# Optimization experiments

Hardware: AMD Instinct MI355X
Metric: run time of the kernel (lower is better)

Reference implementation:

```python
import jax, jax.numpy as jnp
import numpy as np

N_NODES = 100000   # number of graph nodes
N_EDGES = 1000000  # number of edges
D_IN = 64          # input feature dim
D_OUT = 64         # output feature dim
N_RELS = 16        # number of relation types


def setup_inputs() -> dict:
    key = jax.random.key(0)
    k1, k2, k3, k4, k5 = jax.random.split(key, 5)
    feat = jax.random.normal(k1, (N_NODES, D_IN), dtype=jnp.float32)
    weight = jax.random.normal(k2, (N_RELS, D_IN, D_OUT), dtype=jnp.float32) * 0.05
    src = jax.random.randint(k3, (N_EDGES,), 0, N_NODES)
    dst = jax.random.randint(k4, (N_EDGES,), 0, N_NODES)
    etypes = jax.random.randint(k5, (N_EDGES,), 0, N_RELS)
    return {"feat": feat, "weight": weight, "src": src, "dst": dst, "etypes": etypes}


def reference(feat, weight, src, dst, etypes):
    # gather source-node features per edge: h = edges.src['h']
    h = feat[src]                                # [E, d_in]
    n_rels = weight.shape[0]
    e, d_out = h.shape[0], weight.shape[2]

    # gather_mm(h, weight, idx_b=etypes): m_e = h_e @ weight[etypes_e]
    # grouped-GEMM realized as R masked dense GEMMs (R is small, fixed);
    # avoids materializing the [E, d_in, d_out] gathered weight tensor.
    def step(m, rw):
        r, w_r = rw
        mask = jnp.where(etypes == r, 1.0, 0.0).astype(h.dtype)  # [E]
        m = m + mask[:, None] * (h @ w_r)                        # [E, d_out]
        return m, None

    m0 = jnp.zeros((e, d_out), dtype=h.dtype)
    m, _ = jax.lax.scan(step, m0, (jnp.arange(n_rels), weight))

    # update_all(..., fn.sum('m', 'h')): scatter-sum messages to dst nodes
    out = jax.ops.segment_sum(m, dst, num_segments=feat.shape[0])  # [N, d_out]
    return out
```

## Files before the change

kernel.cpp:

```cpp
#include <hip/hip_runtime.h>
#include <hip/hip_bf16.h>
#include <stdint.h>

#define NNODES 100000
#define NEDGES 1000000
#define NRELS 16
#define EPB 2048
#define NB ((NEDGES + EPB - 1) / EPB)
#define PADCAP (NEDGES + NRELS * 64)
#define MAXTILES (PADCAP / 64)
#define NDN NNODES
#define BKT 256
#define NBKT ((NDN + BKT - 1) / BKT)

#define FEAT_BLKS 6250
#define W_BLKS 256
#define SETUP_BLKS (FEAT_BLKS + W_BLKS + NB)
#define SCANS_BLKS (1 + (NBKT + 15) / 16)

#define WS_NEED 157070848ull

using short8  = __attribute__((ext_vector_type(8))) short;
using floatx4 = __attribute__((ext_vector_type(4))) float;
using uintx4  = __attribute__((ext_vector_type(4))) unsigned int;

__device__ __forceinline__ unsigned short f2bf(float f) {
    union { float f; uint32_t u; } v; v.f = f;
    uint32_t u = v.u;
    return (unsigned short)((u + 0x7FFFu + ((u >> 16) & 1u)) >> 16);
}
__device__ __forceinline__ float bf2f(uint32_t u16) {
    union { uint32_t u; float f; } v; v.u = u16 << 16;
    return v.f;
}
__device__ __forceinline__ uint32_t pk2(float a, float b) {
    __hip_bfloat162 h = __float22bfloat162_rn(make_float2(a, b));
    union { __hip_bfloat162 h; uint32_t u; } v; v.h = h;
    return v.u;
}

__global__ void k_setup(const float* __restrict__ feat, const float* __restrict__ W,
                        const int* __restrict__ et, const int* __restrict__ dst,
                        unsigned short* __restrict__ featB, unsigned short* __restrict__ Wt,
                        int* __restrict__ hist16, int* __restrict__ hist391) {
    __shared__ int cnt16[16];
    __shared__ int cnt391[NBKT];
    const int b = blockIdx.x;
    if (b < FEAT_BLKS) {
        int i = (b * 256 + threadIdx.x) * 4;
        const float4 f = *(const float4*)(feat + i);
        ushort4 o;
        o.x = f2bf(f.x); o.y = f2bf(f.y); o.z = f2bf(f.z); o.w = f2bf(f.w);
        *(ushort4*)(featB + i) = o;
    } else if (b < FEAT_BLKS + W_BLKS) {
        int t = (b - FEAT_BLKS) * 256 + threadIdx.x;
        int r = t >> 12, n = (t >> 6) & 63, k = t & 63;
        Wt[t] = f2bf(W[(r << 12) + (k << 6) + n]);
    } else {
        const int bb = b - (FEAT_BLKS + W_BLKS);
        if (threadIdx.x < 16) cnt16[threadIdx.x] = 0;
        for (int t = threadIdx.x; t < NBKT; t += 256) cnt391[t] = 0;
        __syncthreads();
        int start = bb * EPB;
        int end = min(NEDGES, start + EPB);
        for (int i = start + threadIdx.x; i < end; i += 256) {
            atomicAdd(&cnt16[et[i]], 1);
            atomicAdd(&cnt391[dst[i] >> 8], 1);
        }
        __syncthreads();
        if (threadIdx.x < 16) hist16[bb * 16 + threadIdx.x] = cnt16[threadIdx.x];
        for (int t = threadIdx.x; t < NBKT; t += 256)
            hist391[bb * NBKT + t] = cnt391[t];
    }
}

__global__ void __launch_bounds__(1024)
k_scans(const int* __restrict__ hist16, int* __restrict__ bbase16,
        int* __restrict__ Pve,
        const int* __restrict__ hist391, int* __restrict__ bbase391,
        int* __restrict__ bstart) {
    int w = threadIdx.x >> 6;
    int lane = threadIdx.x & 63;
    if (blockIdx.x == 0) {
        __shared__ int s_cnt[16];
        __shared__ int s_P[17];
        int carry = 0;
        for (int c = 0; c < NB; c += 64) {
            int idx = c + lane;
            int v = (idx < NB) ? hist16[idx * 16 + w] : 0;
            int x = v;
            #pragma unroll
            for (int off = 1; off < 64; off <<= 1) {
                int y = __shfl_up(x, off);
                if (lane >= off) x += y;
            }
            if (idx < NB) bbase16[idx * 16 + w] = carry + x - v;
            carry += __shfl(x, 63);
        }
        if (lane == 0) s_cnt[w] = carry;
        __syncthreads();
        if (threadIdx.x == 0) {
            int p = 0;
            for (int r = 0; r < 16; ++r) {
                s_P[r] = p;
                Pve[r] = p;
                Pve[17 + r] = p + s_cnt[r];
                p += (s_cnt[r] + 63) & ~63;
            }
            s_P[16] = p;
            Pve[16] = p;
        }
        __syncthreads();
        int pw = s_P[w];
        for (int idx = lane; idx < NB; idx += 64)
            bbase16[idx * 16 + w] += pw;
    } else {
        int b = (blockIdx.x - 1) * 16 + w;
        if (b >= NBKT) return;
        int carry = 0;
        for (int c = 0; c < NB; c += 64) {
            int idx = c + lane;
            int v = (idx < NB) ? hist391[idx * NBKT + b] : 0;
            int x = v;
            #pragma unroll
            for (int off = 1; off < 64; off <<= 1) {
                int y = __shfl_up(x, off);
                if (lane >= off) x += y;
            }
            if (idx < NB) bbase391[idx * NBKT + b] = carry + x - v;
            carry += __shfl(x, 63);
        }
        if (lane == 0) bstart[b] = carry;
    }
}

__global__ void k_bscanB(int* __restrict__ bstart) {
    __shared__ int wtot[8];
    int t = threadIdx.x;
    int v = (t < NBKT) ? bstart[t] : 0;
    int lane = t & 63, w = t >> 6;
    int x = v;
    #pragma unroll
    for (int off = 1; off < 64; off <<= 1) {
        int y = __shfl_up(x, off);
        if (lane >= off) x += y;
    }
    if (lane == 63) wtot[w] = x;
    __syncthreads();
    int woff = 0;
    for (int i = 0; i < w; ++i) woff += wtot[i];
    if (t < NBKT) bstart[t] = woff + x - v;
    if (t == 511) {
        int total = 0;
        for (int i = 0; i < 8; ++i) total += wtot[i];
        bstart[NBKT] = total;
    }
}

__global__ void k_scatter(const int* __restrict__ et, const int* __restrict__ src,
                          const int* __restrict__ dst, const int* __restrict__ bbase16,
                          const int* __restrict__ bbase391, const int* __restrict__ bstart,
                          int* __restrict__ srcS, int* __restrict__ keyE,
                          unsigned short* __restrict__ dnode) {
    __shared__ int base16[16];
    __shared__ int base391[NBKT];
    if (threadIdx.x < 16) base16[threadIdx.x] = bbase16[blockIdx.x * 16 + threadIdx.x];
    for (int t = threadIdx.x; t < NBKT; t += 256)
        base391[t] = bbase391[blockIdx.x * NBKT + t] + bstart[t];
    __syncthreads();
    int start = blockIdx.x * EPB;
    int end = min(NEDGES, start + EPB);
    for (int i = start + threadIdx.x; i < end; i += 256) {
        int r = et[i];
        int pos = atomicAdd(&base16[r], 1);
        srcS[pos] = src[i];
        int d = dst[i];
        int bp = atomicAdd(&base391[d >> 8], 1);
        keyE[bp] = pos;
        dnode[bp] = (unsigned short)(d & 255);
    }
}

__global__ void __launch_bounds__(256)
k_bsort(const unsigned short* __restrict__ dnode, const int* __restrict__ keyE,
        const int* __restrict__ bstart,
        int* __restrict__ keyS, int* __restrict__ dnstart) {
    __shared__ int cnt[256];
    __shared__ int nodebase[256];
    __shared__ int wtot[4];
    const int b = blockIdx.x;
    const int start = bstart[b], end = bstart[b + 1];
    const int t = threadIdx.x;
    cnt[t] = 0;
    __syncthreads();
    for (int e = start + t; e < end; e += 256)
        atomicAdd(&cnt[dnode[e]], 1);
    __syncthreads();
    int v = cnt[t];
    int lane = t & 63, w = t >> 6;
    int x = v;
    #pragma unroll
    for (int off = 1; off < 64; off <<= 1) {
        int y = __shfl_up(x, off);
        if (lane >= off) x += y;
    }
    if (lane == 63) wtot[w] = x;
    __syncthreads();
    int woff = 0;
    for (int i = 0; i < w; ++i) woff += wtot[i];
    nodebase[t] = woff + x - v;
    cnt[t] = 0;
    __syncthreads();
    dnstart[b * 256 + t] = start + nodebase[t];
    if (b == NBKT - 1 && t == 255) dnstart[NBKT * 256] = end;
    for (int e = start + t; e < end; e += 256) {
        int node = dnode[e];
        int rk = atomicAdd(&cnt[node], 1);
        keyS[start + nodebase[node] + rk] = keyE[e];
    }
}

__global__ void __launch_bounds__(256)
k_computeA(const unsigned short* __restrict__ featB,
           const unsigned short* __restrict__ Wt,
           const int* __restrict__ srcS, const int* __restrict__ Pve,
           unsigned short* __restrict__ msgE) {
    __shared__ float lds[4][16 * 68];
    const int w = threadIdx.x >> 6;
    const int t = blockIdx.x * 4 + w;
    const int base = t * 64;
    const int total = Pve[16];
    if (base >= total) return;
    int r = 0;
    while (base >= Pve[r + 1]) ++r;
    const int validEnd = Pve[17 + r];
    const int lane = threadIdx.x & 63;
    const int quad = lane >> 4;
    const int l16 = lane & 15;

    const unsigned short* wr = Wt + (r << 12);
    short8 bfr[4][2];
    #pragma unroll
    for (int tn = 0; tn < 4; ++tn)
        #pragma unroll
        for (int ks = 0; ks < 2; ++ks)
            bfr[tn][ks] = *(const short8*)(wr + ((tn * 16 + l16) << 6) + ks * 32 + quad * 8);

    const int rr = lane >> 2, seg = lane & 3;
    #pragma unroll
    for (int tm = 0; tm < 4; ++tm) {
        int row = base + tm * 16 + l16;
        int s = (row < validEnd) ? srcS[row] : 0;
        const unsigned short* fp = featB + (s << 6) + quad * 8;
        short8 a0 = *(const short8*)(fp);
        short8 a1 = *(const short8*)(fp + 32);
        #pragma unroll
        for (int tn = 0; tn < 4; ++tn) {
            floatx4 c = {0.f, 0.f, 0.f, 0.f};
            c = __builtin_amdgcn_mfma_f32_16x16x32_bf16(a0, bfr[tn][0], c, 0, 0, 0);
            c = __builtin_amdgcn_mfma_f32_16x16x32_bf16(a1, bfr[tn][1], c, 0, 0, 0);
            #pragma unroll
            for (int j = 0; j < 4; ++j)
                lds[w][(quad * 4 + j) * 68 + tn * 16 + l16] = c[j];
        }
        int grow = base + tm * 16 + rr;
        const float* lp = &lds[w][rr * 68 + seg * 16];
        uintx4 o0, o1;
        o0.x = pk2(lp[0],  lp[1]);  o0.y = pk2(lp[2],  lp[3]);
        o0.z = pk2(lp[4],  lp[5]);  o0.w = pk2(lp[6],  lp[7]);
        o1.x = pk2(lp[8],  lp[9]);  o1.y = pk2(lp[10], lp[11]);
        o1.z = pk2(lp[12], lp[13]); o1.w = pk2(lp[14], lp[15]);
        uintx4* op = (uintx4*)(msgE + (size_t)grow * 64 + seg * 16);
        op[0] = o0;
        op[1] = o1;
    }
}

__global__ void __launch_bounds__(256)
k_reduce(const unsigned short* __restrict__ msgE, const int* __restrict__ keyS,
         const int* __restrict__ dnstart, float* __restrict__ out) {
    int n = blockIdx.x * 4 + (threadIdx.x >> 6);
    if (n >= NDN) return;
    int lane = threadIdx.x & 63;
    int start = dnstart[n];
    int end = dnstart[n + 1];
    int c8 = (lane & 7) * 8;
    float a0 = 0.f, a1 = 0.f, a2 = 0.f, a3 = 0.f;
    float a4 = 0.f, a5 = 0.f, a6 = 0.f, a7 = 0.f;
    for (int row = start + (lane >> 3); row < end; row += 8) {
        int rp = keyS[row];
        uintx4 v = *(const uintx4*)(msgE + (size_t)rp * 64 + c8);
        a0 += bf2f(v.x & 0xffffu); a1 += bf2f(v.x >> 16);
        a2 += bf2f(v.y & 0xffffu); a3 += bf2f(v.y >> 16);
        a4 += bf2f(v.z & 0xffffu); a5 += bf2f(v.z >> 16);
        a6 += bf2f(v.w & 0xffffu); a7 += bf2f(v.w >> 16);
    }
    #pragma unroll
    for (int m = 8; m <= 32; m <<= 1) {
        a0 += __shfl_xor(a0, m); a1 += __shfl_xor(a1, m);
        a2 += __shfl_xor(a2, m); a3 += __shfl_xor(a3, m);
        a4 += __shfl_xor(a4, m); a5 += __shfl_xor(a5, m);
        a6 += __shfl_xor(a6, m); a7 += __shfl_xor(a7, m);
    }
    if (lane < 8) {
        float* op = out + (size_t)n * 64 + lane * 8;
        *(float4*)(op)     = make_float4(a0, a1, a2, a3);
        *(float4*)(op + 4) = make_float4(a4, a5, a6, a7);
    }
}

__global__ void __launch_bounds__(256)
k_fb(const float* __restrict__ feat, const float* __restrict__ W,
     const int* __restrict__ src, const int* __restrict__ dst,
     const int* __restrict__ et, float* __restrict__ out) {
    int e = blockIdx.x * 4 + (threadIdx.x >> 6);
    if (e >= NEDGES) return;
    int c = threadIdx.x & 63;
    int s = src[e], d = dst[e], r = et[e];
    const float* fr = feat + (size_t)s * 64;
    const float* wr = W + ((size_t)r << 12);
    float acc = 0.f;
    for (int k = 0; k < 64; ++k) acc += fr[k] * wr[k * 64 + c];
    atomicAdd(out + (size_t)d * 64 + c, acc);
}

extern "C" void kernel_launch(void* const* d_in, const int* in_sizes, int n_in,
                              void* d_out, int out_size, void* d_ws, size_t ws_size,
                              hipStream_t stream) {
    const float* feat = (const float*)d_in[0];
    const float* W    = (const float*)d_in[1];
    const int* src    = (const int*)d_in[2];
    const int* dst    = (const int*)d_in[3];
    const int* et     = (const int*)d_in[4];
    float* out = (float*)d_out;
    char* ws = (char*)d_ws;

    unsigned short* featB = (unsigned short*)(ws);
    unsigned short* Wt    = (unsigned short*)(ws + 12800000);
    int* hist16   = (int*)(ws + 12931072);
    int* bbase16  = (int*)(ws + 12963840);
    int* Pve      = (int*)(ws + 12996608);
    int* hist391  = (int*)(ws + 12996864);
    int* bbase391 = (int*)(ws + 13764864);
    int* bstart   = (int*)(ws + 14532864);
    unsigned short* dnode = (unsigned short*)(ws + 14534912);
    int* dnstart  = (int*)(ws + 16534912);
    int* keyE     = (int*)(ws + 16935680);
    int* keyS     = (int*)(ws + 20935680);
    int* srcS     = (int*)(ws + 24935680);
    unsigned short* msgE = (unsigned short*)(ws + 28939776);

    if (ws_size >= WS_NEED) {
        k_setup<<<SETUP_BLKS, 256, 0, stream>>>(feat, W, et, dst, featB, Wt,
                                                hist16, hist391);
        k_scans<<<SCANS_BLKS, 1024, 0, stream>>>(hist16, bbase16, Pve, hist391,
                                                 bbase391, bstart);
        k_bscanB<<<1, 512, 0, stream>>>(bstart);
        k_scatter<<<NB, 256, 0, stream>>>(et, src, dst, bbase16, bbase391, bstart,
                                          srcS, keyE, dnode);
        k_bsort<<<NBKT, 256, 0, stream>>>(dnode, keyE, bstart, keyS, dnstart);
        k_computeA<<<(MAXTILES + 3) / 4, 256, 0, stream>>>(featB, Wt, srcS, Pve, msgE);
        k_reduce<<<(NDN + 3) / 4, 256, 0, stream>>>(msgE, keyS, dnstart, out);
    } else {
        hipMemsetAsync(d_out, 0, (size_t)out_size * sizeof(float), stream);
        k_fb<<<(NEDGES + 3) / 4, 256, 0, stream>>>(feat, W, src, dst, et, out);
    }
}
```

Before: 235.3 us.

## Sub-sort edges by source bucket within each relation for gather locality

Edges are now grouped by relation and, within each relation, by 256-node source bucket. The edge histogram and scatter use a composite key, and the scan stage is restructured to compute the per-bucket offsets. The aim is more cache locality for the feature gathers in the grouped GEMM. In exchange, the histograms grow much larger, EPB doubles to shrink them, and the scan and scatter work increases.

```diff
diff --git a/kernel.cpp b/kernel.cpp
--- a/kernel.cpp
+++ b/kernel.cpp
@@ -5,20 +5,23 @@
 #define NNODES 100000
 #define NEDGES 1000000
 #define NRELS 16
-#define EPB 2048
+#define EPB 4096
 #define NB ((NEDGES + EPB - 1) / EPB)
 #define PADCAP (NEDGES + NRELS * 64)
 #define MAXTILES (PADCAP / 64)
 #define NDN NNODES
 #define BKT 256
 #define NBKT ((NDN + BKT - 1) / BKT)
+#define NSB 391
+#define NCB (NRELS * NSB)
 
 #define FEAT_BLKS 6250
 #define W_BLKS 256
 #define SETUP_BLKS (FEAT_BLKS + W_BLKS + NB)
-#define SCANS_BLKS (1 + (NBKT + 15) / 16)
-
-#define WS_NEED 157070848ull
+#define CB_BLKS ((NCB + 15) / 16)
+#define DST_BLKS ((NBKT + 15) / 16)
+
+#define WS_NEED 168522240ull
 
 using short8  = __attribute__((ext_vector_type(8))) short;
 using floatx4 = __attribute__((ext_vector_type(4))) float;
@@ -40,10 +43,11 @@
 }
 
 __global__ void k_setup(const float* __restrict__ feat, const float* __restrict__ W,
-                        const int* __restrict__ et, const int* __restrict__ dst,
+                        const int* __restrict__ et, const int* __restrict__ src,
+                        const int* __restrict__ dst,
                         unsigned short* __restrict__ featB, unsigned short* __restrict__ Wt,
-                        int* __restrict__ hist16, int* __restrict__ hist391) {
-    __shared__ int cnt16[16];
+                        int* __restrict__ hist_cb, int* __restrict__ hist391) {
+    __shared__ int cnt_cb[NCB];
     __shared__ int cnt391[NBKT];
     const int b = blockIdx.x;
     if (b < FEAT_BLKS) {
@@ -58,64 +62,47 @@
         Wt[t] = f2bf(W[(r << 12) + (k << 6) + n]);
     } else {
         const int bb = b - (FEAT_BLKS + W_BLKS);
-        if (threadIdx.x < 16) cnt16[threadIdx.x] = 0;
+        for (int t = threadIdx.x; t < NCB; t += 256) cnt_cb[t] = 0;
         for (int t = threadIdx.x; t < NBKT; t += 256) cnt391[t] = 0;
         __syncthreads();
         int start = bb * EPB;
         int end = min(NEDGES, start + EPB);
         for (int i = start + threadIdx.x; i < end; i += 256) {
-            atomicAdd(&cnt16[et[i]], 1);
+            atomicAdd(&cnt_cb[et[i] * NSB + (src[i] >> 8)], 1);
             atomicAdd(&cnt391[dst[i] >> 8], 1);
         }
         __syncthreads();
-        if (threadIdx.x < 16) hist16[bb * 16 + threadIdx.x] = cnt16[threadIdx.x];
+        for (int t = threadIdx.x; t < NCB; t += 256)
+            hist_cb[bb * NCB + t] = cnt_cb[t];
         for (int t = threadIdx.x; t < NBKT; t += 256)
             hist391[bb * NBKT + t] = cnt391[t];
     }
 }
 
 __global__ void __launch_bounds__(1024)
-k_scans(const int* __restrict__ hist16, int* __restrict__ bbase16,
-        int* __restrict__ Pve,
+k_scanA(const int* __restrict__ hist_cb, int* __restrict__ bbase_cb,
+        int* __restrict__ cbstart,
         const int* __restrict__ hist391, int* __restrict__ bbase391,
         int* __restrict__ bstart) {
-    int w = threadIdx.x >> 6;
-    int lane = threadIdx.x & 63;
-    if (blockIdx.x == 0) {
-        __shared__ int s_cnt[16];
-        __shared__ int s_P[17];
+    int w = threadIdx.x >> 6, lane = threadIdx.x & 63;
+    if (blockIdx.x < CB_BLKS) {
+        int b = blockIdx.x * 16 + w;
         int carry = 0;
         for (int c = 0; c < NB; c += 64) {
             int idx = c + lane;
-            int v = (idx < NB) ? hist16[idx * 16 + w] : 0;
+            int v = (idx < NB) ? hist_cb[idx * NCB + b] : 0;
             int x = v;
             #pragma unroll
             for (int off = 1; off < 64; off <<= 1) {
                 int y = __shfl_up(x, off);
                 if (lane >= off) x += y;
             }
-            if (idx < NB) bbase16[idx * 16 + w] = carry + x - v;
+            if (idx < NB) bbase_cb[idx * NCB + b] = carry + x - v;
             carry += __shfl(x, 63);
         }
-        if (lane == 0) s_cnt[w] = carry;
-        __syncthreads();
-        if (threadIdx.x == 0) {
-            int p = 0;
-            for (int r = 0; r < 16; ++r) {
-                s_P[r] = p;
-                Pve[r] = p;
-                Pve[17 + r] = p + s_cnt[r];
-                p += (s_cnt[r] + 63) & ~63;
-            }
-            s_P[16] = p;
-            Pve[16] = p;
-        }
-        __syncthreads();
-        int pw = s_P[w];
-        for (int idx = lane; idx < NB; idx += 64)
-            bbase16[idx * 16 + w] += pw;
+        if (lane == 0) cbstart[b] = carry;
     } else {
-        int b = (blockIdx.x - 1) * 16 + w;
+        int b = (blockIdx.x - CB_BLKS) * 16 + w;
         if (b >= NBKT) return;
         int carry = 0;
         for (int c = 0; c < NB; c += 64) {
@@ -134,11 +121,44 @@
     }
 }
 
-__global__ void k_bscanB(int* __restrict__ bstart) {
-    __shared__ int wtot[8];
+__global__ void __launch_bounds__(1024)
+k_scanB(int* __restrict__ cbstart, int* __restrict__ Pve, int* __restrict__ bstart) {
+    __shared__ int s_cnt[16];
+    __shared__ int s_P[17];
+    __shared__ int wtot[16];
+    int w = threadIdx.x >> 6, lane = threadIdx.x & 63;
+    int carry = 0;
+    for (int c = 0; c < NSB; c += 64) {
+        int idx = c + lane;
+        int v = (idx < NSB) ? cbstart[w * NSB + idx] : 0;
+        int x = v;
+        #pragma unroll
+        for (int off = 1; off < 64; off <<= 1) {
+            int y = __shfl_up(x, off);
+            if (lane >= off) x += y;
+        }
+        if (idx < NSB) cbstart[w * NSB + idx] = carry + x - v;
+        carry += __shfl(x, 63);
+    }
+    if (lane == 0) s_cnt[w] = carry;
+    __syncthreads();
+    if (threadIdx.x == 0) {
+        int p = 0;
+        for (int r = 0; r < 16; ++r) {
+            s_P[r] = p;
+            Pve[r] = p;
+            Pve[17 + r] = p + s_cnt[r];
+            p += (s_cnt[r] + 63) & ~63;
+        }
+        Pve[16] = p;
+    }
+    __syncthreads();
+    int pw = s_P[w];
+    for (int idx = lane; idx < NSB; idx += 64)
+        cbstart[w * NSB + idx] += pw;
+    __syncthreads();
     int t = threadIdx.x;
     int v = (t < NBKT) ? bstart[t] : 0;
-    int lane = t & 63, w = t >> 6;
     int x = v;
     #pragma unroll
     for (int off = 1; off < 64; off <<= 1) {
@@ -150,30 +170,33 @@
     int woff = 0;
     for (int i = 0; i < w; ++i) woff += wtot[i];
     if (t < NBKT) bstart[t] = woff + x - v;
-    if (t == 511) {
+    if (t == 1023) {
         int total = 0;
-        for (int i = 0; i < 8; ++i) total += wtot[i];
+        for (int i = 0; i < 16; ++i) total += wtot[i];
         bstart[NBKT] = total;
     }
 }
 
-__global__ void k_scatter(const int* __restrict__ et, const int* __restrict__ src,
-                          const int* __restrict__ dst, const int* __restrict__ bbase16,
-                          const int* __restrict__ bbase391, const int* __restrict__ bstart,
-                          int* __restrict__ srcS, int* __restrict__ keyE,
-                          unsigned short* __restrict__ dnode) {
-    __shared__ int base16[16];
+__global__ void __launch_bounds__(256)
+k_scatter(const int* __restrict__ et, const int* __restrict__ src,
+          const int* __restrict__ dst,
+          const int* __restrict__ bbase_cb, const int* __restrict__ cbstart,
+          const int* __restrict__ bbase391, const int* __restrict__ bstart,
+          int* __restrict__ srcS, int* __restrict__ keyE,
+          unsigned short* __restrict__ dnode) {
+    __shared__ int base_cb[NCB];
     __shared__ int base391[NBKT];
-    if (threadIdx.x < 16) base16[threadIdx.x] = bbase16[blockIdx.x * 16 + threadIdx.x];
+    for (int t = threadIdx.x; t < NCB; t += 256)
+        base_cb[t] = bbase_cb[blockIdx.x * NCB + t] + cbstart[t];
     for (int t = threadIdx.x; t < NBKT; t += 256)
         base391[t] = bbase391[blockIdx.x * NBKT + t] + bstart[t];
     __syncthreads();
     int start = blockIdx.x * EPB;
     int end = min(NEDGES, start + EPB);
     for (int i = start + threadIdx.x; i < end; i += 256) {
-        int r = et[i];
-        int pos = atomicAdd(&base16[r], 1);
-        srcS[pos] = src[i];
+        int s = src[i];
+        int pos = atomicAdd(&base_cb[et[i] * NSB + (s >> 8)], 1);
+        srcS[pos] = s;
         int d = dst[i];
         int bp = atomicAdd(&base391[d >> 8], 1);
         keyE[bp] = pos;
@@ -337,27 +360,28 @@
 
     unsigned short* featB = (unsigned short*)(ws);
     unsigned short* Wt    = (unsigned short*)(ws + 12800000);
-    int* hist16   = (int*)(ws + 12931072);
-    int* bbase16  = (int*)(ws + 12963840);
-    int* Pve      = (int*)(ws + 12996608);
-    int* hist391  = (int*)(ws + 12996864);
-    int* bbase391 = (int*)(ws + 13764864);
-    int* bstart   = (int*)(ws + 14532864);
-    unsigned short* dnode = (unsigned short*)(ws + 14534912);
-    int* dnstart  = (int*)(ws + 16534912);
-    int* keyE     = (int*)(ws + 16935680);
-    int* keyS     = (int*)(ws + 20935680);
-    int* srcS     = (int*)(ws + 24935680);
-    unsigned short* msgE = (unsigned short*)(ws + 28939776);
+    int* hist_cb  = (int*)(ws + 12931072);
+    int* bbase_cb = (int*)(ws + 19061952);
+    int* cbstart  = (int*)(ws + 25192832);
+    int* Pve      = (int*)(ws + 25217856);
+    int* hist391  = (int*)(ws + 25218112);
+    int* bbase391 = (int*)(ws + 25601344);
+    int* bstart   = (int*)(ws + 25984576);
+    unsigned short* dnode = (unsigned short*)(ws + 25986624);
+    int* dnstart  = (int*)(ws + 27986624);
+    int* keyE     = (int*)(ws + 28387072);
+    int* keyS     = (int*)(ws + 32387072);
+    int* srcS     = (int*)(ws + 36387072);
+    unsigned short* msgE = (unsigned short*)(ws + 40391168);
 
     if (ws_size >= WS_NEED) {
-        k_setup<<<SETUP_BLKS, 256, 0, stream>>>(feat, W, et, dst, featB, Wt,
-                                                hist16, hist391);
-        k_scans<<<SCANS_BLKS, 1024, 0, stream>>>(hist16, bbase16, Pve, hist391,
-                                                 bbase391, bstart);
-        k_bscanB<<<1, 512, 0, stream>>>(bstart);
-        k_scatter<<<NB, 256, 0, stream>>>(et, src, dst, bbase16, bbase391, bstart,
-                                          srcS, keyE, dnode);
+        k_setup<<<SETUP_BLKS, 256, 0, stream>>>(feat, W, et, src, dst, featB, Wt,
+                                                hist_cb, hist391);
+        k_scanA<<<CB_BLKS + DST_BLKS, 1024, 0, stream>>>(hist_cb, bbase_cb, cbstart,
+                                                         hist391, bbase391, bstart);
+        k_scanB<<<1, 1024, 0, stream>>>(cbstart, Pve, bstart);
+        k_scatter<<<NB, 256, 0, stream>>>(et, src, dst, bbase_cb, cbstart,
+                                          bbase391, bstart, srcS, keyE, dnode);
         k_bsort<<<NBKT, 256, 0, stream>>>(dnode, keyE, bstart, keyS, dnstart);
         k_computeA<<<(MAXTILES + 3) / 4, 256, 0, stream>>>(featB, Wt, srcS, Pve, msgE);
         k_reduce<<<(NDN + 3) / 4, 256, 0, stream>>>(msgE, keyS, dnstart, out);
```

After: 251.9 us. +7.1%, slower.
